# Performance work log

Measured on AMD Instinct MI355X. Metric: run time of the kernel, lower is better.

## Reference

```python
import jax, jax.numpy as jnp
import numpy as np

N_NODES = 50000
N_EDGES = 800000
D_FEAT = 64
HIDDEN = 64
OUT = 2


def setup_inputs() -> dict:
    key = jax.random.key(0)
    ks = jax.random.split(key, 12)
    s = 1.0 / np.sqrt(D_FEAT)
    h = 1.0 / np.sqrt(HIDDEN)
    return {
        "x": jax.random.normal(ks[0], (N_NODES, D_FEAT), jnp.float32),
        "edge_index": jax.random.randint(ks[1], (2, N_EDGES), 0, N_NODES, jnp.int64),
        # SAGEConv layer 1: lin_l (aggregated neighbors, with bias), lin_r (root, no bias)
        "W1l": jax.random.uniform(ks[2], (D_FEAT, HIDDEN), jnp.float32, -s, s),
        "b1": jnp.zeros((HIDDEN,), jnp.float32),
        "W1r": jax.random.uniform(ks[3], (D_FEAT, HIDDEN), jnp.float32, -s, s),
        # SAGEConv layer 2
        "W2l": jax.random.uniform(ks[4], (HIDDEN, HIDDEN), jnp.float32, -h, h),
        "b2": jnp.zeros((HIDDEN,), jnp.float32),
        "W2r": jax.random.uniform(ks[5], (HIDDEN, HIDDEN), jnp.float32, -h, h),
        # final Linear
        "Wlin": jax.random.uniform(ks[6], (HIDDEN, OUT), jnp.float32, -h, h),
        "blin": jnp.zeros((OUT,), jnp.float32),
    }


def _sage_conv(h, src, dst, n_nodes, Wl, bl, Wr):
    # mean-aggregate source features at target nodes (PyG SAGEConv, aggr='mean')
    msgs = h[src]  # [E, d] gather
    agg = jax.ops.segment_sum(msgs, dst, num_segments=n_nodes)
    cnt = jax.ops.segment_sum(jnp.ones((src.shape[0],), h.dtype), dst, num_segments=n_nodes)
    agg = agg / jnp.maximum(cnt, 1.0)[:, None]
    return agg @ Wl + bl + h @ Wr


def reference(x, edge_index, W1l, b1, W1r, W2l, b2, W2r, Wlin, blin):
    src, dst = edge_index[0], edge_index[1]
    n = x.shape[0]
    h1 = jax.nn.relu(_sage_conv(x, src, dst, n, W1l, b1, W1r))
    h2 = jax.nn.relu(_sage_conv(h1, src, dst, n, W2l, b2, W2r))
    return h2 @ Wlin + blin
```

## Files before the change

kernel.cpp:

```cpp
#include <hip/hip_runtime.h>
#include <hip/hip_fp16.h>

namespace {

constexpr int N = 50000;
constexpr int E = 800000;
constexpr int D = 64;
constexpr int TN = 128;
constexpr int APAD = 132;
constexpr int CAP = 64;
constexpr int NR = 256;
constexpr int RW = 196;
constexpr int CAPR = 3584;
constexpr int EPB = 2048;

__device__ __forceinline__ void gemm_tile(float (*a_s)[APAD],
                                          const float* __restrict__ A,
                                          const float* __restrict__ Wl,
                                          const float* __restrict__ Wr,
                                          const float* __restrict__ bias,
                                          __half* __restrict__ P,
                                          float* __restrict__ Q, int n, int blk) {
  int tid = threadIdx.x;
  int base = blk * TN;

  const float4* A4 = (const float4*)A;
  for (int i = tid; i < TN * 16; i += 256) {
    int node = i & 127;
    int kq = i >> 7;
    int gn = base + node;
    float4 v = (gn < n) ? A4[(size_t)gn * 16 + kq] : make_float4(0.f, 0.f, 0.f, 0.f);
    a_s[kq * 4 + 0][node] = v.x;
    a_s[kq * 4 + 1][node] = v.y;
    a_s[kq * 4 + 2][node] = v.z;
    a_s[kq * 4 + 3][node] = v.w;
  }
  __syncthreads();

  int ng = tid & 15;
  int cg = tid >> 4;

  float acc[8][8];
#pragma unroll
  for (int i = 0; i < 8; ++i)
#pragma unroll
    for (int j = 0; j < 8; ++j) acc[i][j] = (j < 4) ? 0.0f : bias[cg * 4 + (j - 4)];

#pragma unroll 4
  for (int k = 0; k < D; ++k) {
    float4 a0 = *(const float4*)&a_s[k][ng * 4];
    float4 a1 = *(const float4*)&a_s[k][64 + ng * 4];
    float4 w0 = *(const float4*)&Wl[k * D + cg * 4];
    float4 w1 = *(const float4*)&Wr[k * D + cg * 4];
    float av[8] = {a0.x, a0.y, a0.z, a0.w, a1.x, a1.y, a1.z, a1.w};
    float wv[8] = {w0.x, w0.y, w0.z, w0.w, w1.x, w1.y, w1.z, w1.w};
#pragma unroll
    for (int i = 0; i < 8; ++i)
#pragma unroll
      for (int j = 0; j < 8; ++j) acc[i][j] = fmaf(av[i], wv[j], acc[i][j]);
  }

  uint2* P2 = (uint2*)P;
  float4* Q4 = (float4*)Q;
#pragma unroll
  for (int i = 0; i < 8; ++i) {
    int gn = base + ((i < 4) ? (ng * 4 + i) : (64 + ng * 4 + (i - 4)));
    if (gn < n) {
      __half2 p01 = __floats2half2_rn(acc[i][0], acc[i][1]);
      __half2 p23 = __floats2half2_rn(acc[i][2], acc[i][3]);
      uint2 pu;
      pu.x = *reinterpret_cast<const unsigned*>(&p01);
      pu.y = *reinterpret_cast<const unsigned*>(&p23);
      P2[(size_t)gn * 16 + cg] = pu;
      Q4[(size_t)gn * 16 + cg] = make_float4(acc[i][4], acc[i][5], acc[i][6], acc[i][7]);
    }
  }
}

__device__ __forceinline__ void place_phase1(const int* __restrict__ src,
                                             const int* __restrict__ dst,
                                             int* __restrict__ cursor,
                                             unsigned int* __restrict__ staging,
                                             int nE, int blk) {
  __shared__ int hist[NR];
  __shared__ int hist2[NR];
  __shared__ int rbase[NR];
  int t = threadIdx.x;
  for (int i = t; i < NR; i += 256) { hist[i] = 0; hist2[i] = 0; }
  __syncthreads();

  int e0 = blk * EPB + t * 8;
  int rr[8];
  unsigned dlo[8];
#pragma unroll
  for (int j = 0; j < 8; ++j) {
    int e = e0 + j;
    if (e < nE) {
      unsigned d = (unsigned)dst[e];
      unsigned r = d / RW;
      rr[j] = (int)r;
      dlo[j] = d - r * RW;
      atomicAdd(&hist[r], 1);
    } else {
      rr[j] = -1;
    }
  }
  __syncthreads();
  if (t < NR) rbase[t] = hist[t] ? atomicAdd(&cursor[t], hist[t]) : 0;
  __syncthreads();
#pragma unroll
  for (int j = 0; j < 8; ++j) {
    if (rr[j] >= 0) {
      unsigned s = (unsigned)src[e0 + j];
      int q = atomicAdd(&hist2[rr[j]], 1);
      int off = rbase[rr[j]] + q;
      if (off < CAPR)
        staging[(size_t)rr[j] * CAPR + off] = (s << 8) | dlo[j];
    }
  }
}

__global__ __launch_bounds__(256) void gemm_place_kernel(
    const float* __restrict__ A, const float* __restrict__ Wl,
    const float* __restrict__ Wr, const float* __restrict__ bias,
    __half* __restrict__ P, float* __restrict__ Q, int n, int nGB,
    const int* __restrict__ src, const int* __restrict__ dst,
    int* __restrict__ cursor, unsigned int* __restrict__ staging, int nE) {
  __shared__ float a_s[D][APAD];
  if ((int)blockIdx.x < nGB) {
    gemm_tile(a_s, A, Wl, Wr, bias, P, Q, n, blockIdx.x);
  } else {
    place_phase1(src, dst, cursor, staging, nE, (int)blockIdx.x - nGB);
  }
}

__global__ __launch_bounds__(256) void place_phase2(
    const unsigned int* __restrict__ staging, const int* __restrict__ cursor,
    unsigned short* __restrict__ bucket, int* __restrict__ cntg) {
  __shared__ int lcnt[RW];
  int t = threadIdx.x;
  int r = blockIdx.x;
  for (int i = t; i < RW; i += 256) lcnt[i] = 0;
  __syncthreads();

  int M = min(cursor[r], CAPR);
  const unsigned int* st = staging + (size_t)r * CAPR;
  int nbase = r * RW;
  for (int i = t; i < M; i += 256) {
    unsigned v = st[i];
    int nl = (int)(v & 255u);
    unsigned s = v >> 8;
    int p = atomicAdd(&lcnt[nl], 1);
    if (p < CAP) bucket[(size_t)(nbase + nl) * CAP + p] = (unsigned short)s;
  }
  __syncthreads();
  for (int i = t; i < RW; i += 256) {
    int node = nbase + i;
    if (node < N) cntg[node] = lcnt[i];
  }
}

__global__ __launch_bounds__(256) void gemm_kernel(const float* __restrict__ A,
                                                   const float* __restrict__ Wl,
                                                   const float* __restrict__ Wr,
                                                   const float* __restrict__ bias,
                                                   __half* __restrict__ P,
                                                   float* __restrict__ Q, int n) {
  __shared__ float a_s[D][APAD];
  gemm_tile(a_s, A, Wl, Wr, bias, P, Q, n, blockIdx.x);
}

template <bool FINAL>
__global__ __launch_bounds__(256) void gather_kernel(
    const __half* __restrict__ P, const float* __restrict__ Q,
    const unsigned short* __restrict__ bucket, const int* __restrict__ cntg,
    const float* __restrict__ Wlin, const float* __restrict__ blin,
    float* __restrict__ hout, float* __restrict__ outp, int n) {
  int tid = threadIdx.x;
  int lane = tid & 63;
  int sub = tid >> 6;
  int node = blockIdx.x * 4 + sub;
  if (node >= n) return;

  int ct = cntg[node];
  float scale = 1.0f / fmaxf((float)ct, 1.0f);
  int c = min(ct, CAP);

  int r = lane >> 4;
  int c4 = lane & 15;
  const uint2* P2 = (const uint2*)P;
  const float4* Q4 = (const float4*)Q;
  const unsigned short* slots = bucket + (size_t)node * CAP;

  float4 a = make_float4(0.f, 0.f, 0.f, 0.f);
  for (int i0 = r; i0 < c; i0 += 16) {
    int cm = c - 1;
    int s0 = slots[i0];
    int s1 = slots[min(i0 + 4, cm)];
    int s2 = slots[min(i0 + 8, cm)];
    int s3 = slots[min(i0 + 12, cm)];
    uint2 z; z.x = 0u; z.y = 0u;
    uint2 u0 = P2[(size_t)s0 * 16 + c4];
    uint2 u1 = z, u2 = z, u3 = z;
    if (i0 + 4 < c) u1 = P2[(size_t)s1 * 16 + c4];
    if (i0 + 8 < c) u2 = P2[(size_t)s2 * 16 + c4];
    if (i0 + 12 < c) u3 = P2[(size_t)s3 * 16 + c4];
#pragma unroll
    for (int j = 0; j < 4; ++j) {
      uint2 u = (j == 0) ? u0 : (j == 1) ? u1 : (j == 2) ? u2 : u3;
      float2 fa = __half22float2(*reinterpret_cast<const __half2*>(&u.x));
      float2 fb = __half22float2(*reinterpret_cast<const __half2*>(&u.y));
      a.x += fa.x; a.y += fa.y; a.z += fb.x; a.w += fb.y;
    }
  }

  a.x += __shfl_xor(a.x, 16, 64); a.y += __shfl_xor(a.y, 16, 64);
  a.z += __shfl_xor(a.z, 16, 64); a.w += __shfl_xor(a.w, 16, 64);
  a.x += __shfl_xor(a.x, 32, 64); a.y += __shfl_xor(a.y, 32, 64);
  a.z += __shfl_xor(a.z, 32, 64); a.w += __shfl_xor(a.w, 32, 64);

  float4 q = Q4[(size_t)node * 16 + c4];
  float4 h;
  h.x = fmaxf(fmaf(a.x, scale, q.x), 0.f);
  h.y = fmaxf(fmaf(a.y, scale, q.y), 0.f);
  h.z = fmaxf(fmaf(a.z, scale, q.z), 0.f);
  h.w = fmaxf(fmaf(a.w, scale, q.w), 0.f);

  if (!FINAL) {
    if (r == 0) ((float4*)hout)[(size_t)node * 16 + c4] = h;
  } else {
    const float2* W2 = (const float2*)Wlin;
    float2 w0 = W2[c4 * 4 + 0], w1 = W2[c4 * 4 + 1];
    float2 w2 = W2[c4 * 4 + 2], w3 = W2[c4 * 4 + 3];
    float a0 = h.x * w0.x + h.y * w1.x + h.z * w2.x + h.w * w3.x;
    float a1 = h.x * w0.y + h.y * w1.y + h.z * w2.y + h.w * w3.y;
#pragma unroll
    for (int ofs = 8; ofs > 0; ofs >>= 1) {
      a0 += __shfl_xor(a0, ofs, 64);
      a1 += __shfl_xor(a1, ofs, 64);
    }
    if (lane == 0) {
      outp[(size_t)node * 2 + 0] = a0 + blin[0];
      outp[(size_t)node * 2 + 1] = a1 + blin[1];
    }
  }
}

}

extern "C" void kernel_launch(void* const* d_in, const int* in_sizes, int n_in,
                              void* d_out, int out_size, void* d_ws, size_t ws_size,
                              hipStream_t stream) {
  const float* x    = (const float*)d_in[0];
  const int*   ei   = (const int*)d_in[1];
  const float* W1l  = (const float*)d_in[2];
  const float* b1   = (const float*)d_in[3];
  const float* W1r  = (const float*)d_in[4];
  const float* W2l  = (const float*)d_in[5];
  const float* b2   = (const float*)d_in[6];
  const float* W2r  = (const float*)d_in[7];
  const float* Wlin = (const float*)d_in[8];
  const float* blin = (const float*)d_in[9];
  float* out = (float*)d_out;

  char* ws = (char*)d_ws;
  size_t p = 0;
  float*          h    = (float*)(ws + p);          p += (size_t)N * D * 4;
  __half*         P    = (__half*)(ws + p);         p += (size_t)N * D * 2;
  float*          Q    = (float*)(ws + p);          p += (size_t)N * D * 4;
  unsigned short* bkt  = (unsigned short*)(ws + p); p += (size_t)N * CAP * 2;
  int*            cntg = (int*)(ws + p);            p += (size_t)((N * 4 + 255) & ~255);
  unsigned int*   stg  = (unsigned int*)(ws + p);   p += (size_t)NR * CAPR * 4;
  int*            cur  = (int*)(ws + p);            p += (size_t)NR * 4;

  const int* src = ei;
  const int* dst = ei + E;

  const int GB = (N + TN - 1) / TN;
  const int PB = (E + EPB - 1) / EPB;

  hipMemsetAsync(cur, 0, (size_t)NR * sizeof(int), stream);

  gemm_place_kernel<<<GB + PB, 256, 0, stream>>>(
      x, W1l, W1r, b1, P, Q, N, GB, src, dst, cur, stg, E);

  place_phase2<<<NR, 256, 0, stream>>>(stg, cur, bkt, cntg);

  gather_kernel<false><<<(N + 3) / 4, 256, 0, stream>>>(
      P, Q, bkt, cntg, nullptr, nullptr, h, nullptr, N);

  gemm_kernel<<<GB, 256, 0, stream>>>(h, W2l, W2r, b2, P, Q, N);

  gather_kernel<true><<<(N + 3) / 4, 256, 0, stream>>>(
      P, Q, bkt, cntg, Wlin, blin, nullptr, out, N);
}
```

Measured before the change: 120.5 us.

## Fuse layer-1 gather into layer-2 GEMM and store root term in fp16

The layer-1 neighbor gather is merged into the layer-2 GEMM kernel: each block gathers 128 nodes straight into shared memory and runs the GEMM on them, so the fp32 hidden buffer is never written and read back and one launch is dropped. The root-term Q buffer moves from fp32 to fp16, halving its traffic, and separate P/Q buffers per layer avoid read-after-write hazards. In exchange the fused kernel has only about 391 blocks, so the latency-bound gather phase runs at much lower parallelism than the old 12500-block gather. The fp16 Q also adds rounding error.

```diff
diff --git a/kernel.cpp b/kernel.cpp
--- a/kernel.cpp
+++ b/kernel.cpp
@@ -14,16 +14,60 @@
 constexpr int CAPR = 3584;
 constexpr int EPB = 2048;
 
-__device__ __forceinline__ void gemm_tile(float (*a_s)[APAD],
-                                          const float* __restrict__ A,
+__device__ __forceinline__ uint2 pack4h(float a, float b, float c, float d) {
+  __half2 lo = __floats2half2_rn(a, b);
+  __half2 hi = __floats2half2_rn(c, d);
+  uint2 u;
+  u.x = *reinterpret_cast<unsigned*>(&lo);
+  u.y = *reinterpret_cast<unsigned*>(&hi);
+  return u;
+}
+
+__device__ __forceinline__ void gemm_core(float (*a_s)[APAD],
                                           const float* __restrict__ Wl,
                                           const float* __restrict__ Wr,
                                           const float* __restrict__ bias,
                                           __half* __restrict__ P,
-                                          float* __restrict__ Q, int n, int blk) {
+                                          __half* __restrict__ Q, int n, int base) {
   int tid = threadIdx.x;
-  int base = blk * TN;
-
+  int ng = tid & 15;
+  int cg = tid >> 4;
+
+  float acc[8][8];
+#pragma unroll
+  for (int i = 0; i < 8; ++i)
+#pragma unroll
+    for (int j = 0; j < 8; ++j) acc[i][j] = (j < 4) ? 0.0f : bias[cg * 4 + (j - 4)];
+
+#pragma unroll 4
+  for (int k = 0; k < D; ++k) {
+    float4 a0 = *(const float4*)&a_s[k][ng * 4];
+    float4 a1 = *(const float4*)&a_s[k][64 + ng * 4];
+    float4 w0 = *(const float4*)&Wl[k * D + cg * 4];
+    float4 w1 = *(const float4*)&Wr[k * D + cg * 4];
+    float av[8] = {a0.x, a0.y, a0.z, a0.w, a1.x, a1.y, a1.z, a1.w};
+    float wv[8] = {w0.x, w0.y, w0.z, w0.w, w1.x, w1.y, w1.z, w1.w};
+#pragma unroll
+    for (int i = 0; i < 8; ++i)
+#pragma unroll
+      for (int j = 0; j < 8; ++j) acc[i][j] = fmaf(av[i], wv[j], acc[i][j]);
+  }
+
+  uint2* Pv = (uint2*)P;
+  uint2* Qv = (uint2*)Q;
+#pragma unroll
+  for (int i = 0; i < 8; ++i) {
+    int gn = base + ((i < 4) ? (ng * 4 + i) : (64 + ng * 4 + (i - 4)));
+    if (gn < n) {
+      Pv[(size_t)gn * 16 + cg] = pack4h(acc[i][0], acc[i][1], acc[i][2], acc[i][3]);
+      Qv[(size_t)gn * 16 + cg] = pack4h(acc[i][4], acc[i][5], acc[i][6], acc[i][7]);
+    }
+  }
+}
+
+__device__ __forceinline__ void stage_a(float (*a_s)[APAD],
+                                        const float* __restrict__ A, int n, int base) {
+  int tid = threadIdx.x;
   const float4* A4 = (const float4*)A;
   for (int i = tid; i < TN * 16; i += 256) {
     int node = i & 127;
@@ -36,45 +80,6 @@
     a_s[kq * 4 + 3][node] = v.w;
   }
   __syncthreads();
-
-  int ng = tid & 15;
-  int cg = tid >> 4;
-
-  float acc[8][8];
-#pragma unroll
-  for (int i = 0; i < 8; ++i)
-#pragma unroll
-    for (int j = 0; j < 8; ++j) acc[i][j] = (j < 4) ? 0.0f : bias[cg * 4 + (j - 4)];
-
-#pragma unroll 4
-  for (int k = 0; k < D; ++k) {
-    float4 a0 = *(const float4*)&a_s[k][ng * 4];
-    float4 a1 = *(const float4*)&a_s[k][64 + ng * 4];
-    float4 w0 = *(const float4*)&Wl[k * D + cg * 4];
-    float4 w1 = *(const float4*)&Wr[k * D + cg * 4];
-    float av[8] = {a0.x, a0.y, a0.z, a0.w, a1.x, a1.y, a1.z, a1.w};
-    float wv[8] = {w0.x, w0.y, w0.z, w0.w, w1.x, w1.y, w1.z, w1.w};
-#pragma unroll
-    for (int i = 0; i < 8; ++i)
-#pragma unroll
-      for (int j = 0; j < 8; ++j) acc[i][j] = fmaf(av[i], wv[j], acc[i][j]);
-  }
-
-  uint2* P2 = (uint2*)P;
-  float4* Q4 = (float4*)Q;
-#pragma unroll
-  for (int i = 0; i < 8; ++i) {
-    int gn = base + ((i < 4) ? (ng * 4 + i) : (64 + ng * 4 + (i - 4)));
-    if (gn < n) {
-      __half2 p01 = __floats2half2_rn(acc[i][0], acc[i][1]);
-      __half2 p23 = __floats2half2_rn(acc[i][2], acc[i][3]);
-      uint2 pu;
-      pu.x = *reinterpret_cast<const unsigned*>(&p01);
-      pu.y = *reinterpret_cast<const unsigned*>(&p23);
-      P2[(size_t)gn * 16 + cg] = pu;
-      Q4[(size_t)gn * 16 + cg] = make_float4(acc[i][4], acc[i][5], acc[i][6], acc[i][7]);
-    }
-  }
 }
 
 __device__ __forceinline__ void place_phase1(const int* __restrict__ src,
@@ -123,12 +128,13 @@
 __global__ __launch_bounds__(256) void gemm_place_kernel(
     const float* __restrict__ A, const float* __restrict__ Wl,
     const float* __restrict__ Wr, const float* __restrict__ bias,
-    __half* __restrict__ P, float* __restrict__ Q, int n, int nGB,
+    __half* __restrict__ P, __half* __restrict__ Q, int n, int nGB,
     const int* __restrict__ src, const int* __restrict__ dst,
     int* __restrict__ cursor, unsigned int* __restrict__ staging, int nE) {
   __shared__ float a_s[D][APAD];
   if ((int)blockIdx.x < nGB) {
-    gemm_tile(a_s, A, Wl, Wr, bias, P, Q, n, blockIdx.x);
+    stage_a(a_s, A, n, blockIdx.x * TN);
+    gemm_core(a_s, Wl, Wr, bias, P, Q, n, blockIdx.x * TN);
   } else {
     place_phase1(src, dst, cursor, staging, nE, (int)blockIdx.x - nGB);
   }
@@ -160,36 +166,14 @@
   }
 }
 
-__global__ __launch_bounds__(256) void gemm_kernel(const float* __restrict__ A,
-                                                   const float* __restrict__ Wl,
-                                                   const float* __restrict__ Wr,
-                                                   const float* __restrict__ bias,
-                                                   __half* __restrict__ P,
-                                                   float* __restrict__ Q, int n) {
-  __shared__ float a_s[D][APAD];
-  gemm_tile(a_s, A, Wl, Wr, bias, P, Q, n, blockIdx.x);
-}
-
-template <bool FINAL>
-__global__ __launch_bounds__(256) void gather_kernel(
-    const __half* __restrict__ P, const float* __restrict__ Q,
-    const unsigned short* __restrict__ bucket, const int* __restrict__ cntg,
-    const float* __restrict__ Wlin, const float* __restrict__ blin,
-    float* __restrict__ hout, float* __restrict__ outp, int n) {
-  int tid = threadIdx.x;
-  int lane = tid & 63;
-  int sub = tid >> 6;
-  int node = blockIdx.x * 4 + sub;
-  if (node >= n) return;
-
+__device__ __forceinline__ float4 gather_node(const uint2* __restrict__ Pv,
+                                              const uint2* __restrict__ Qv,
+                                              const unsigned short* __restrict__ bucket,
+                                              const int* __restrict__ cntg,
+                                              int node, int r, int c4) {
   int ct = cntg[node];
   float scale = 1.0f / fmaxf((float)ct, 1.0f);
   int c = min(ct, CAP);
-
-  int r = lane >> 4;
-  int c4 = lane & 15;
-  const uint2* P2 = (const uint2*)P;
-  const float4* Q4 = (const float4*)Q;
   const unsigned short* slots = bucket + (size_t)node * CAP;
 
   float4 a = make_float4(0.f, 0.f, 0.f, 0.f);
@@ -200,11 +184,11 @@
     int s2 = slots[min(i0 + 8, cm)];
     int s3 = slots[min(i0 + 12, cm)];
     uint2 z; z.x = 0u; z.y = 0u;
-    uint2 u0 = P2[(size_t)s0 * 16 + c4];
+    uint2 u0 = Pv[(size_t)s0 * 16 + c4];
     uint2 u1 = z, u2 = z, u3 = z;
-    if (i0 + 4 < c) u1 = P2[(size_t)s1 * 16 + c4];
-    if (i0 + 8 < c) u2 = P2[(size_t)s2 * 16 + c4];
-    if (i0 + 12 < c) u3 = P2[(size_t)s3 * 16 + c4];
+    if (i0 + 4 < c) u1 = Pv[(size_t)s1 * 16 + c4];
+    if (i0 + 8 < c) u2 = Pv[(size_t)s2 * 16 + c4];
+    if (i0 + 12 < c) u3 = Pv[(size_t)s3 * 16 + c4];
 #pragma unroll
     for (int j = 0; j < 4; ++j) {
       uint2 u = (j == 0) ? u0 : (j == 1) ? u1 : (j == 2) ? u2 : u3;
@@ -213,36 +197,81 @@
       a.x += fa.x; a.y += fa.y; a.z += fb.x; a.w += fb.y;
     }
   }
-
   a.x += __shfl_xor(a.x, 16, 64); a.y += __shfl_xor(a.y, 16, 64);
   a.z += __shfl_xor(a.z, 16, 64); a.w += __shfl_xor(a.w, 16, 64);
   a.x += __shfl_xor(a.x, 32, 64); a.y += __shfl_xor(a.y, 32, 64);
   a.z += __shfl_xor(a.z, 32, 64); a.w += __shfl_xor(a.w, 32, 64);
 
-  float4 q = Q4[(size_t)node * 16 + c4];
+  uint2 qv = Qv[(size_t)node * 16 + c4];
+  float2 qa = __half22float2(*reinterpret_cast<const __half2*>(&qv.x));
+  float2 qb = __half22float2(*reinterpret_cast<const __half2*>(&qv.y));
   float4 h;
-  h.x = fmaxf(fmaf(a.x, scale, q.x), 0.f);
-  h.y = fmaxf(fmaf(a.y, scale, q.y), 0.f);
-  h.z = fmaxf(fmaf(a.z, scale, q.z), 0.f);
-  h.w = fmaxf(fmaf(a.w, scale, q.w), 0.f);
-
-  if (!FINAL) {
-    if (r == 0) ((float4*)hout)[(size_t)node * 16 + c4] = h;
-  } else {
-    const float2* W2 = (const float2*)Wlin;
-    float2 w0 = W2[c4 * 4 + 0], w1 = W2[c4 * 4 + 1];
-    float2 w2 = W2[c4 * 4 + 2], w3 = W2[c4 * 4 + 3];
-    float a0 = h.x * w0.x + h.y * w1.x + h.z * w2.x + h.w * w3.x;
-    float a1 = h.x * w0.y + h.y * w1.y + h.z * w2.y + h.w * w3.y;
-#pragma unroll
-    for (int ofs = 8; ofs > 0; ofs >>= 1) {
-      a0 += __shfl_xor(a0, ofs, 64);
-      a1 += __shfl_xor(a1, ofs, 64);
-    }
-    if (lane == 0) {
-      outp[(size_t)node * 2 + 0] = a0 + blin[0];
-      outp[(size_t)node * 2 + 1] = a1 + blin[1];
-    }
+  h.x = fmaxf(fmaf(a.x, scale, qa.x), 0.f);
+  h.y = fmaxf(fmaf(a.y, scale, qa.y), 0.f);
+  h.z = fmaxf(fmaf(a.z, scale, qb.x), 0.f);
+  h.w = fmaxf(fmaf(a.w, scale, qb.y), 0.f);
+  return h;
+}
+
+__global__ __launch_bounds__(256) void gather_gemm_kernel(
+    const __half* __restrict__ P1, const __half* __restrict__ Q1,
+    const unsigned short* __restrict__ bucket, const int* __restrict__ cntg,
+    const float* __restrict__ W2l, const float* __restrict__ W2r,
+    const float* __restrict__ b2,
+    __half* __restrict__ P2, __half* __restrict__ Q2, int n) {
+  __shared__ float a_s[D][APAD];
+  int tid = threadIdx.x;
+  int lane = tid & 63;
+  int wave = tid >> 6;
+  int base = blockIdx.x * TN;
+  int r = lane >> 4;
+  int c4 = lane & 15;
+  const uint2* Pv = (const uint2*)P1;
+  const uint2* Qv = (const uint2*)Q1;
+
+  for (int nl = wave; nl < TN; nl += 4) {
+    int node = base + nl;
+    float4 h = make_float4(0.f, 0.f, 0.f, 0.f);
+    if (node < n) h = gather_node(Pv, Qv, bucket, cntg, node, r, c4);
+    if (r == 0) {
+      a_s[4 * c4 + 0][nl] = h.x;
+      a_s[4 * c4 + 1][nl] = h.y;
+      a_s[4 * c4 + 2][nl] = h.z;
+      a_s[4 * c4 + 3][nl] = h.w;
+    }
+  }
+  __syncthreads();
+  gemm_core(a_s, W2l, W2r, b2, P2, Q2, n, base);
+}
+
+__global__ __launch_bounds__(256) void gather_final_kernel(
+    const __half* __restrict__ P, const __half* __restrict__ Q,
+    const unsigned short* __restrict__ bucket, const int* __restrict__ cntg,
+    const float* __restrict__ Wlin, const float* __restrict__ blin,
+    float* __restrict__ outp, int n) {
+  int tid = threadIdx.x;
+  int lane = tid & 63;
+  int sub = tid >> 6;
+  int node = blockIdx.x * 4 + sub;
+  if (node >= n) return;
+
+  int r = lane >> 4;
+  int c4 = lane & 15;
+  float4 h = gather_node((const uint2*)P, (const uint2*)Q, bucket, cntg, node, r, c4);
+
+  const float2* W2 = (const float2*)Wlin;
+  float2 w0 = W2[c4 * 4 + 0], w1 = W2[c4 * 4 + 1];
+  float2 w2 = W2[c4 * 4 + 2], w3 = W2[c4 * 4 + 3];
+  float a0 = h.x * w0.x + h.y * w1.x + h.z * w2.x + h.w * w3.x;
+  float a1 = h.x * w0.y + h.y * w1.y + h.z * w2.y + h.w * w3.y;
+#pragma unroll
+  for (int ofs = 8; ofs > 0; ofs >>= 1) {
+    a0 += __shfl_xor(a0, ofs, 64);
+    a1 += __shfl_xor(a1, ofs, 64);
+  }
+  if (lane == 0) {
+    outp[(size_t)node * 2 + 0] = a0 + blin[0];
+    outp[(size_t)node * 2 + 1] = a1 + blin[1];
   }
 }
 
@@ -265,9 +294,10 @@
 
   char* ws = (char*)d_ws;
   size_t p = 0;
-  float*          h    = (float*)(ws + p);          p += (size_t)N * D * 4;
-  __half*         P    = (__half*)(ws + p);         p += (size_t)N * D * 2;
-  float*          Q    = (float*)(ws + p);          p += (size_t)N * D * 4;
+  __half*         P1   = (__half*)(ws + p);         p += (size_t)N * D * 2;
+  __half*         Q1   = (__half*)(ws + p);         p += (size_t)N * D * 2;
+  __half*         P2   = (__half*)(ws + p);         p += (size_t)N * D * 2;
+  __half*         Q2   = (__half*)(ws + p);         p += (size_t)N * D * 2;
   unsigned short* bkt  = (unsigned short*)(ws + p); p += (size_t)N * CAP * 2;
   int*            cntg = (int*)(ws + p);            p += (size_t)((N * 4 + 255) & ~255);
   unsigned int*   stg  = (unsigned int*)(ws + p);   p += (size_t)NR * CAPR * 4;
@@ -282,15 +312,13 @@
   hipMemsetAsync(cur, 0, (size_t)NR * sizeof(int), stream);
 
   gemm_place_kernel<<<GB + PB, 256, 0, stream>>>(
-      x, W1l, W1r, b1, P, Q, N, GB, src, dst, cur, stg, E);
+      x, W1l, W1r, b1, P1, Q1, N, GB, src, dst, cur, stg, E);
 
   place_phase2<<<NR, 256, 0, stream>>>(stg, cur, bkt, cntg);
 
-  gather_kernel<false><<<(N + 3) / 4, 256, 0, stream>>>(
-      P, Q, bkt, cntg, nullptr, nullptr, h, nullptr, N);
-
-  gemm_kernel<<<GB, 256, 0, stream>>>(h, W2l, W2r, b2, P, Q, N);
-
-  gather_kernel<true><<<(N + 3) / 4, 256, 0, stream>>>(
-      P, Q, bkt, cntg, Wlin, blin, nullptr, out, N);
-}
+  gather_gemm_kernel<<<GB, 256, 0, stream>>>(
+      P1, Q1, bkt, cntg, W2l, W2r, b2, P2, Q2, N);
+
+  gather_final_kernel<<<(N + 3) / 4, 256, 0, stream>>>(
+      P2, Q2, bkt, cntg, Wlin, blin, out, N);
+}
```

New measurement: 159.2 us. 32.2% more time.
